# Kernel tuning notes

Hardware: AMD Instinct MI355X
Metric: run time of the kernel (lower is better)

## Reference

```python
import jax, jax.numpy as jnp
import numpy as np

B, H, W, Z = 2, 256, 256, 256


def _shift_zero(x, axis, offset):
    """Shift x along `axis` by `offset`, zero-filling the vacated slab.
    offset=-1: out[i] = x[i-1]; offset=+1: out[i] = x[i+1]."""
    pad = [(0, 0)] * x.ndim
    idx = [slice(None)] * x.ndim
    if offset == -1:
        pad[axis] = (1, 0)
        idx[axis] = slice(0, x.shape[axis])
    else:
        pad[axis] = (0, 1)
        idx[axis] = slice(1, x.shape[axis] + 1)
    return jnp.pad(x, pad)[tuple(idx)]


def apply_7pt_stencil(x, coeff):
    # x: [B,H,W,Z], coeff: [B,H,W,7] broadcast over Z
    west = _shift_zero(x, 2, -1)
    east = _shift_zero(x, 2, 1)
    south = _shift_zero(x, 1, -1)
    north = _shift_zero(x, 1, 1)
    bottom = _shift_zero(x, 3, -1)
    top = _shift_zero(x, 3, 1)
    c = coeff[..., None, :]  # [B,H,W,1,7]
    return (c[..., 0] * west + c[..., 1] * east + c[..., 2] * south
            + c[..., 3] * north + c[..., 4] * bottom + c[..., 5] * top
            + c[..., 6] * x)


def setup_inputs() -> dict:
    key = jax.random.key(0)
    k1, k2, k3 = jax.random.split(key, 3)
    x = jax.random.normal(k1, (B, H, W, Z), dtype=jnp.float32)
    coeff = jax.random.uniform(k2, (B, H, W, 7), dtype=jnp.float32)
    ref = jax.random.normal(k3, (B, H, W, Z), dtype=jnp.float32)
    return {"x": x, "coeff": coeff, "ref": ref}


def reference(x, coeff, ref):
    output = apply_7pt_stencil(x, coeff)
    error = (output - ref).astype(jnp.float32)
    loss = jnp.mean(error * error)
    max_abs_error = jnp.max(jnp.abs(error))
    return loss, output, max_abs_error
```

## Files before the change

kernel.cpp:

```cpp
#include <hip/hip_runtime.h>

#define HH 256
#define WW 256
#define ZZ 256
#define BBH 512
#define LSTRIDE (WW * ZZ)
#define NROWS (BBH * WW)
#define NELEM ((long long)NROWS * ZZ)

#define SEGW 8
#define NTW (WW / SEGW)
#define NPAIR (BBH / 2)
#define NSEG (NPAIR * NTW)
#define WPB 4
#define NBLK (NSEG / WPB)

typedef float vf4 __attribute__((ext_vector_type(4)));

__device__ __forceinline__ vf4 ld4(const float* p) { return *(const vf4*)p; }
__device__ __forceinline__ vf4 ldnt4(const float* p) {
    return __builtin_nontemporal_load((const vf4*)p);
}

__device__ __forceinline__ void store_row(float* rowp, vf4 o, int lane) {
    const float nx = __shfl_down(o.x, 1);
    const float ny = __shfl_down(o.y, 1);
    const float nz = __shfl_down(o.z, 1);
    if (lane < 63) {
        vf4 st = {o.w, nx, ny, nz};
        __builtin_nontemporal_store(st, (vf4*)(rowp + 4 * (lane + 1)));
    }
    if (lane == 0) {
        __builtin_nontemporal_store(o.x, rowp + 1);
        __builtin_nontemporal_store(o.y, rowp + 2);
        __builtin_nontemporal_store(o.z, rowp + 3);
    }
    if (lane == 63) __builtin_nontemporal_store(o.w, rowp + ZZ);
}

__global__ __launch_bounds__(256) void stencil7_kernel(
    const float* __restrict__ x, const float* __restrict__ coeff,
    const float* __restrict__ ref, float* __restrict__ outD,
    float* __restrict__ part_sum, float* __restrict__ part_max)
{
    const int tid  = threadIdx.x;
    const int k    = tid >> 6;
    const int lane = tid & 63;
    const int seg  = __builtin_amdgcn_readfirstlane(blockIdx.x * WPB + k);
    const int p    = seg >> 5;
    const int wt   = seg & (NTW - 1);
    const int bh0  = p * 2;
    const int w0   = wt * SEGW;
    const int h0   = bh0 & (HH - 1);
    const bool hasS = (h0 > 0);
    const bool hasN = (h0 != HH - 2);
    const long long SOFF = hasS ? -(long long)LSTRIDE : 0;
    const long long NOFF = hasN ? 2LL * LSTRIDE : (long long)LSTRIDE;
    const int lo = lane << 2;

    const float* px0  = x   + (long long)(bh0 * WW + w0) * ZZ + lo;
    const float* px1  = px0 + LSTRIDE;
    const float* prf0 = ref + (long long)(bh0 * WW + w0) * ZZ + lo;
    const float* prf1 = prf0 + LSTRIDE;
    const float* pc0  = coeff + 7LL * (bh0 * WW + w0);
    const float* pc1  = pc0 + 7 * WW;
    float* prow0 = outD + (long long)(bh0 * WW + w0) * ZZ;
    float* prow1 = prow0 + LSTRIDE;

    const vf4 z4 = {0.f, 0.f, 0.f, 0.f};

    vf4 cw0, cw1;
    if (w0 > 0) { cw0 = ld4(px0 - ZZ); cw1 = ld4(px1 - ZZ); }
    else        { cw0 = z4;            cw1 = z4; }
    vf4 c00 = ld4(px0);           vf4 c10 = ld4(px1);
    vf4 c01 = ld4(px0 + ZZ);      vf4 c11 = ld4(px1 + ZZ);
    vf4 sC  = ld4(px0 + SOFF);    vf4 nC  = ld4(px0 + NOFF);
    vf4 rf0 = ldnt4(prf0);        vf4 rf1 = ldnt4(prf1);
    float k0 = pc0[0], k1 = pc0[1], k2 = hasS ? pc0[2] : 0.f, k3 = pc0[3],
          k4 = pc0[4], k5 = pc0[5], k6 = pc0[6];
    float j0 = pc1[0], j1 = pc1[1], j2 = pc1[2], j3 = hasN ? pc1[3] : 0.f,
          j4 = pc1[4], j5 = pc1[5], j6 = pc1[6];

    float acc_s = 0.f, acc_m = 0.f;

    #pragma unroll
    for (int i = 0; i < SEGW - 1; ++i) {
        int ce = w0 + i + 2; if (ce > WW - 1) ce = WW - 1;
        const long long ceo = (long long)(ce - w0) * ZZ;
        vf4 c0n = ld4(px0 + ceo);
        vf4 c1n = ld4(px1 + ceo);
        const long long r1o = (long long)(i + 1) * ZZ;
        vf4 sN  = ld4(px0 + r1o + SOFF);
        vf4 nN  = ld4(px0 + r1o + NOFF);
        vf4 rf0n = ldnt4(prf0 + r1o);
        vf4 rf1n = ldnt4(prf1 + r1o);
        const float* qc0 = pc0 + 7 * (i + 1);
        const float* qc1 = pc1 + 7 * (i + 1);
        const float m0 = qc0[0], m1 = qc0[1], m2 = hasS ? qc0[2] : 0.f,
                    m3 = qc0[3], m4 = qc0[4], m5 = qc0[5], m6 = qc0[6];
        const float n0 = qc1[0], n1 = qc1[1], n2 = qc1[2],
                    n3 = hasN ? qc1[3] : 0.f, n4 = qc1[4], n5 = qc1[5], n6 = qc1[6];

        {
            float bm1 = __shfl_up(c00.w, 1);
            if (lane == 0) bm1 = 0.f;
            float tp1 = __shfl_down(c00.x, 1);
            if (lane == 63) tp1 = 0.f;
            const vf4 bot = {bm1, c00.x, c00.y, c00.z};
            const vf4 top = {c00.y, c00.z, c00.w, tp1};
            const vf4 o = k0*cw0 + k1*c01 + k2*sC + k3*c10 + k4*bot + k5*top + k6*c00;
            store_row(prow0 + (long long)i * ZZ, o, lane);
            const vf4 e = o - rf0;
            acc_s += e.x*e.x + e.y*e.y + e.z*e.z + e.w*e.w;
            acc_m  = fmaxf(acc_m, fmaxf(fmaxf(fabsf(e.x), fabsf(e.y)),
                                        fmaxf(fabsf(e.z), fabsf(e.w))));
        }
        {
            float bm1 = __shfl_up(c10.w, 1);
            if (lane == 0) bm1 = 0.f;
            float tp1 = __shfl_down(c10.x, 1);
            if (lane == 63) tp1 = 0.f;
            const vf4 bot = {bm1, c10.x, c10.y, c10.z};
            const vf4 top = {c10.y, c10.z, c10.w, tp1};
            const vf4 o = j0*cw1 + j1*c11 + j2*c00 + j3*nC + j4*bot + j5*top + j6*c10;
            store_row(prow1 + (long long)i * ZZ, o, lane);
            const vf4 e = o - rf1;
            acc_s += e.x*e.x + e.y*e.y + e.z*e.z + e.w*e.w;
            acc_m  = fmaxf(acc_m, fmaxf(fmaxf(fabsf(e.x), fabsf(e.y)),
                                        fmaxf(fabsf(e.z), fabsf(e.w))));
        }

        cw0 = c00; c00 = c01; c01 = c0n;
        cw1 = c10; c10 = c11; c11 = c1n;
        sC = sN; nC = nN; rf0 = rf0n; rf1 = rf1n;
        k0 = m0; k1 = m1; k2 = m2; k3 = m3; k4 = m4; k5 = m5; k6 = m6;
        j0 = n0; j1 = n1; j2 = n2; j3 = n3; j4 = n4; j5 = n5; j6 = n6;
    }

    {
        const int i = SEGW - 1;
        if (w0 + i == WW - 1) { k1 = 0.f; j1 = 0.f; }
        {
            float bm1 = __shfl_up(c00.w, 1);
            if (lane == 0) bm1 = 0.f;
            float tp1 = __shfl_down(c00.x, 1);
            if (lane == 63) tp1 = 0.f;
            const vf4 bot = {bm1, c00.x, c00.y, c00.z};
            const vf4 top = {c00.y, c00.z, c00.w, tp1};
            const vf4 o = k0*cw0 + k1*c01 + k2*sC + k3*c10 + k4*bot + k5*top + k6*c00;
            store_row(prow0 + (long long)i * ZZ, o, lane);
            const vf4 e = o - rf0;
            acc_s += e.x*e.x + e.y*e.y + e.z*e.z + e.w*e.w;
            acc_m  = fmaxf(acc_m, fmaxf(fmaxf(fabsf(e.x), fabsf(e.y)),
                                        fmaxf(fabsf(e.z), fabsf(e.w))));
        }
        {
            float bm1 = __shfl_up(c10.w, 1);
            if (lane == 0) bm1 = 0.f;
            float tp1 = __shfl_down(c10.x, 1);
            if (lane == 63) tp1 = 0.f;
            const vf4 bot = {bm1, c10.x, c10.y, c10.z};
            const vf4 top = {c10.y, c10.z, c10.w, tp1};
            const vf4 o = j0*cw1 + j1*c11 + j2*c00 + j3*nC + j4*bot + j5*top + j6*c10;
            store_row(prow1 + (long long)i * ZZ, o, lane);
            const vf4 e = o - rf1;
            acc_s += e.x*e.x + e.y*e.y + e.z*e.z + e.w*e.w;
            acc_m  = fmaxf(acc_m, fmaxf(fmaxf(fabsf(e.x), fabsf(e.y)),
                                        fmaxf(fabsf(e.z), fabsf(e.w))));
        }
    }

    #pragma unroll
    for (int off = 32; off > 0; off >>= 1) {
        acc_s += __shfl_down(acc_s, off);
        acc_m  = fmaxf(acc_m, __shfl_down(acc_m, off));
    }
    __shared__ float ss[WPB];
    __shared__ float sm[WPB];
    if (lane == 0) { ss[k] = acc_s; sm[k] = acc_m; }
    __syncthreads();
    if (tid == 0) {
        part_sum[blockIdx.x] = ss[0] + ss[1] + ss[2] + ss[3];
        part_max[blockIdx.x] = fmaxf(fmaxf(sm[0], sm[1]), fmaxf(sm[2], sm[3]));
    }
}

__global__ __launch_bounds__(256) void finalize_kernel(
    const float* __restrict__ part_sum, const float* __restrict__ part_max,
    float* __restrict__ loss_out, float* __restrict__ amax_out)
{
    const int tid  = threadIdx.x;
    const int wave = tid >> 6;
    const int lane = tid & 63;

    double s = 0.0;
    float  m = 0.f;
    for (int i = tid; i < NBLK; i += 256) {
        s += (double)part_sum[i];
        m  = fmaxf(m, part_max[i]);
    }
    #pragma unroll
    for (int off = 32; off > 0; off >>= 1) {
        s += __shfl_down(s, off);
        m  = fmaxf(m, __shfl_down(m, off));
    }
    __shared__ double ds[4];
    __shared__ float  dm[4];
    if (lane == 0) { ds[wave] = s; dm[wave] = m; }
    __syncthreads();
    if (tid == 0) {
        const double S = ds[0] + ds[1] + ds[2] + ds[3];
        const float  M = fmaxf(fmaxf(dm[0], dm[1]), fmaxf(dm[2], dm[3]));
        *loss_out = (float)(S / (double)NELEM);
        *amax_out = M;
    }
}

extern "C" void kernel_launch(void* const* d_in, const int* in_sizes, int n_in,
                              void* d_out, int out_size, void* d_ws, size_t ws_size,
                              hipStream_t stream) {
    const float* x     = (const float*)d_in[0];
    const float* coeff = (const float*)d_in[1];
    const float* ref   = (const float*)d_in[2];

    float* outf = (float*)d_out;
    float* loss_out = outf;
    float* amax_out = outf + 1 + NELEM;

    float* part_sum = (float*)d_ws;
    float* part_max = part_sum + NBLK;

    stencil7_kernel<<<dim3(NBLK), dim3(256), 0, stream>>>(
        x, coeff, ref, outf, part_sum, part_max);
    finalize_kernel<<<dim3(1), dim3(256), 0, stream>>>(
        part_sum, part_max, loss_out, amax_out);
}
```

Before: 74.49 us.

## Convert stencil kernel to persistent grid with atomic work-stealing task queue

```diff
diff --git a/kernel.cpp b/kernel.cpp
--- a/kernel.cpp
+++ b/kernel.cpp
@@ -13,7 +13,8 @@
 #define NPAIR (BBH / 2)
 #define NSEG (NPAIR * NTW)
 #define WPB 4
-#define NBLK (NSEG / WPB)
+#define NTASK (NSEG / WPB)
+#define GRIDP 1280
 
 typedef float vf4 __attribute__((ext_vector_type(4)));
 
@@ -41,147 +42,150 @@
 __global__ __launch_bounds__(256) void stencil7_kernel(
     const float* __restrict__ x, const float* __restrict__ coeff,
     const float* __restrict__ ref, float* __restrict__ outD,
+    unsigned int* __restrict__ ctr,
     float* __restrict__ part_sum, float* __restrict__ part_max)
 {
+    __shared__ int s_task;
     const int tid  = threadIdx.x;
     const int k    = tid >> 6;
     const int lane = tid & 63;
-    const int seg  = __builtin_amdgcn_readfirstlane(blockIdx.x * WPB + k);
-    const int p    = seg >> 5;
-    const int wt   = seg & (NTW - 1);
-    const int bh0  = p * 2;
-    const int w0   = wt * SEGW;
-    const int h0   = bh0 & (HH - 1);
-    const bool hasS = (h0 > 0);
-    const bool hasN = (h0 != HH - 2);
-    const long long SOFF = hasS ? -(long long)LSTRIDE : 0;
-    const long long NOFF = hasN ? 2LL * LSTRIDE : (long long)LSTRIDE;
-    const int lo = lane << 2;
-
-    const float* px0  = x   + (long long)(bh0 * WW + w0) * ZZ + lo;
-    const float* px1  = px0 + LSTRIDE;
-    const float* prf0 = ref + (long long)(bh0 * WW + w0) * ZZ + lo;
-    const float* prf1 = prf0 + LSTRIDE;
-    const float* pc0  = coeff + 7LL * (bh0 * WW + w0);
-    const float* pc1  = pc0 + 7 * WW;
-    float* prow0 = outD + (long long)(bh0 * WW + w0) * ZZ;
-    float* prow1 = prow0 + LSTRIDE;
-
+    const int lo   = lane << 2;
     const vf4 z4 = {0.f, 0.f, 0.f, 0.f};
 
-    vf4 cw0, cw1;
-    if (w0 > 0) { cw0 = ld4(px0 - ZZ); cw1 = ld4(px1 - ZZ); }
-    else        { cw0 = z4;            cw1 = z4; }
-    vf4 c00 = ld4(px0);           vf4 c10 = ld4(px1);
-    vf4 c01 = ld4(px0 + ZZ);      vf4 c11 = ld4(px1 + ZZ);
-    vf4 sC  = ld4(px0 + SOFF);    vf4 nC  = ld4(px0 + NOFF);
-    vf4 rf0 = ldnt4(prf0);        vf4 rf1 = ldnt4(prf1);
-    float k0 = pc0[0], k1 = pc0[1], k2 = hasS ? pc0[2] : 0.f, k3 = pc0[3],
-          k4 = pc0[4], k5 = pc0[5], k6 = pc0[6];
-    float j0 = pc1[0], j1 = pc1[1], j2 = pc1[2], j3 = hasN ? pc1[3] : 0.f,
-          j4 = pc1[4], j5 = pc1[5], j6 = pc1[6];
-
-    float acc_s = 0.f, acc_m = 0.f;
-
-    #pragma unroll
-    for (int i = 0; i < SEGW - 1; ++i) {
-        int ce = w0 + i + 2; if (ce > WW - 1) ce = WW - 1;
-        const long long ceo = (long long)(ce - w0) * ZZ;
-        vf4 c0n = ld4(px0 + ceo);
-        vf4 c1n = ld4(px1 + ceo);
-        const long long r1o = (long long)(i + 1) * ZZ;
-        vf4 sN  = ld4(px0 + r1o + SOFF);
-        vf4 nN  = ld4(px0 + r1o + NOFF);
-        vf4 rf0n = ldnt4(prf0 + r1o);
-        vf4 rf1n = ldnt4(prf1 + r1o);
-        const float* qc0 = pc0 + 7 * (i + 1);
-        const float* qc1 = pc1 + 7 * (i + 1);
-        const float m0 = qc0[0], m1 = qc0[1], m2 = hasS ? qc0[2] : 0.f,
-                    m3 = qc0[3], m4 = qc0[4], m5 = qc0[5], m6 = qc0[6];
-        const float n0 = qc1[0], n1 = qc1[1], n2 = qc1[2],
-                    n3 = hasN ? qc1[3] : 0.f, n4 = qc1[4], n5 = qc1[5], n6 = qc1[6];
+    int task = blockIdx.x;
+    while (task < NTASK) {
+        const int seg  = __builtin_amdgcn_readfirstlane(task * WPB + k);
+        const int p    = seg >> 5;
+        const int wt   = seg & (NTW - 1);
+        const int bh0  = p * 2;
+        const int w0   = wt * SEGW;
+        const int h0   = bh0 & (HH - 1);
+        const bool hasS = (h0 > 0);
+        const bool hasN = (h0 != HH - 2);
+        const long long SOFF = hasS ? -(long long)LSTRIDE : 0;
+        const long long NOFF = hasN ? 2LL * LSTRIDE : (long long)LSTRIDE;
+
+        const float* px0  = x   + (long long)(bh0 * WW + w0) * ZZ + lo;
+        const float* px1  = px0 + LSTRIDE;
+        const float* prf0 = ref + (long long)(bh0 * WW + w0) * ZZ + lo;
+        const float* prf1 = prf0 + LSTRIDE;
+        const float* pc0  = coeff + 7LL * (bh0 * WW + w0);
+        const float* pc1  = pc0 + 7 * WW;
+        float* prow0 = outD + (long long)(bh0 * WW + w0) * ZZ;
+        float* prow1 = prow0 + LSTRIDE;
+
+        vf4 cw0, cw1;
+        if (w0 > 0) { cw0 = ld4(px0 - ZZ); cw1 = ld4(px1 - ZZ); }
+        else        { cw0 = z4;            cw1 = z4; }
+        vf4 c00 = ld4(px0);           vf4 c10 = ld4(px1);
+        vf4 c01 = ld4(px0 + ZZ);      vf4 c11 = ld4(px1 + ZZ);
+        vf4 sC  = ld4(px0 + SOFF);    vf4 nC  = ld4(px0 + NOFF);
+        vf4 rf0 = ldnt4(prf0);        vf4 rf1 = ldnt4(prf1);
+        float k0 = pc0[0], k1 = pc0[1], k2 = hasS ? pc0[2] : 0.f, k3 = pc0[3],
+              k4 = pc0[4], k5 = pc0[5], k6 = pc0[6];
+        float j0 = pc1[0], j1 = pc1[1], j2 = pc1[2], j3 = hasN ? pc1[3] : 0.f,
+              j4 = pc1[4], j5 = pc1[5], j6 = pc1[6];
+
+        float acc_s = 0.f, acc_m = 0.f;
+
+        #pragma unroll
+        for (int i = 0; i < SEGW - 1; ++i) {
+            int ce = w0 + i + 2; if (ce > WW - 1) ce = WW - 1;
+            const long long ceo = (long long)(ce - w0) * ZZ;
+            vf4 c0n = ld4(px0 + ceo);
+            vf4 c1n = ld4(px1 + ceo);
+            const long long r1o = (long long)(i + 1) * ZZ;
+            vf4 sN  = ld4(px0 + r1o + SOFF);
+            vf4 nN  = ld4(px0 + r1o + NOFF);
+            vf4 rf0n = ldnt4(prf0 + r1o);
+            vf4 rf1n = ldnt4(prf1 + r1o);
+            const float* qc0 = pc0 + 7 * (i + 1);
+            const float* qc1 = pc1 + 7 * (i + 1);
+            const float m0 = qc0[0], m1 = qc0[1], m2 = hasS ? qc0[2] : 0.f,
+                        m3 = qc0[3], m4 = qc0[4], m5 = qc0[5], m6 = qc0[6];
+            const float n0 = qc1[0], n1 = qc1[1], n2 = qc1[2],
+                        n3 = hasN ? qc1[3] : 0.f, n4 = qc1[4], n5 = qc1[5], n6 = qc1[6];
+
+            {
+                float bm1 = __shfl_up(c00.w, 1);
+                if (lane == 0) bm1 = 0.f;
+                float tp1 = __shfl_down(c00.x, 1);
+                if (lane == 63) tp1 = 0.f;
+                const vf4 bot = {bm1, c00.x, c00.y, c00.z};
+                const vf4 top = {c00.y, c00.z, c00.w, tp1};
+                const vf4 o = k0*cw0 + k1*c01 + k2*sC + k3*c10 + k4*bot + k5*top + k6*c00;
+                store_row(prow0 + (long long)i * ZZ, o, lane);
+                const vf4 e = o - rf0;
+                acc_s += e.x*e.x + e.y*e.y + e.z*e.z + e.w*e.w;
+                acc_m  = fmaxf(acc_m, fmaxf(fmaxf(fabsf(e.x), fabsf(e.y)),
+                                            fmaxf(fabsf(e.z), fabsf(e.w))));
+            }
+            {
+                float bm1 = __shfl_up(c10.w, 1);
+                if (lane == 0) bm1 = 0.f;
+                float tp1 = __shfl_down(c10.x, 1);
+                if (lane == 63) tp1 = 0.f;
+                const vf4 bot = {bm1, c10.x, c10.y, c10.z};
+                const vf4 top = {c10.y, c10.z, c10.w, tp1};
+                const vf4 o = j0*cw1 + j1*c11 + j2*c00 + j3*nC + j4*bot + j5*top + j6*c10;
+                store_row(prow1 + (long long)i * ZZ, o, lane);
+                const vf4 e = o - rf1;
+                acc_s += e.x*e.x + e.y*e.y + e.z*e.z + e.w*e.w;
+                acc_m  = fmaxf(acc_m, fmaxf(fmaxf(fabsf(e.x), fabsf(e.y)),
+                                            fmaxf(fabsf(e.z), fabsf(e.w))));
+            }
+
+            cw0 = c00; c00 = c01; c01 = c0n;
+            cw1 = c10; c10 = c11; c11 = c1n;
+            sC = sN; nC = nN; rf0 = rf0n; rf1 = rf1n;
+            k0 = m0; k1 = m1; k2 = m2; k3 = m3; k4 = m4; k5 = m5; k6 = m6;
+            j0 = n0; j1 = n1; j2 = n2; j3 = n3; j4 = n4; j5 = n5; j6 = n6;
+        }
 
         {
-            float bm1 = __shfl_up(c00.w, 1);
-            if (lane == 0) bm1 = 0.f;
-            float tp1 = __shfl_down(c00.x, 1);
-            if (lane == 63) tp1 = 0.f;
-            const vf4 bot = {bm1, c00.x, c00.y, c00.z};
-            const vf4 top = {c00.y, c00.z, c00.w, tp1};
-            const vf4 o = k0*cw0 + k1*c01 + k2*sC + k3*c10 + k4*bot + k5*top + k6*c00;
-            store_row(prow0 + (long long)i * ZZ, o, lane);
-            const vf4 e = o - rf0;
-            acc_s += e.x*e.x + e.y*e.y + e.z*e.z + e.w*e.w;
-            acc_m  = fmaxf(acc_m, fmaxf(fmaxf(fabsf(e.x), fabsf(e.y)),
-                                        fmaxf(fabsf(e.z), fabsf(e.w))));
+            const int i = SEGW - 1;
+            if (w0 + i == WW - 1) { k1 = 0.f; j1 = 0.f; }
+            {
+                float bm1 = __shfl_up(c00.w, 1);
+                if (lane == 0) bm1 = 0.f;
+                float tp1 = __shfl_down(c00.x, 1);
+                if (lane == 63) tp1 = 0.f;
+                const vf4 bot = {bm1, c00.x, c00.y, c00.z};
+                const vf4 top = {c00.y, c00.z, c00.w, tp1};
+                const vf4 o = k0*cw0 + k1*c01 + k2*sC + k3*c10 + k4*bot + k5*top + k6*c00;
+                store_row(prow0 + (long long)i * ZZ, o, lane);
+                const vf4 e = o - rf0;
+                acc_s += e.x*e.x + e.y*e.y + e.z*e.z + e.w*e.w;
+                acc_m  = fmaxf(acc_m, fmaxf(fmaxf(fabsf(e.x), fabsf(e.y)),
+                                            fmaxf(fabsf(e.z), fabsf(e.w))));
+            }
+            {
+                float bm1 = __shfl_up(c10.w, 1);
+                if (lane == 0) bm1 = 0.f;
+                float tp1 = __shfl_down(c10.x, 1);
+                if (lane == 63) tp1 = 0.f;
+                const vf4 bot = {bm1, c10.x, c10.y, c10.z};
+                const vf4 top = {c10.y, c10.z, c10.w, tp1};
+                const vf4 o = j0*cw1 + j1*c11 + j2*c00 + j3*nC + j4*bot + j5*top + j6*c10;
+                store_row(prow1 + (long long)i * ZZ, o, lane);
+                const vf4 e = o - rf1;
+                acc_s += e.x*e.x + e.y*e.y + e.z*e.z + e.w*e.w;
+                acc_m  = fmaxf(acc_m, fmaxf(fmaxf(fabsf(e.x), fabsf(e.y)),
+                                            fmaxf(fabsf(e.z), fabsf(e.w))));
+            }
         }
-        {
-            float bm1 = __shfl_up(c10.w, 1);
-            if (lane == 0) bm1 = 0.f;
-            float tp1 = __shfl_down(c10.x, 1);
-            if (lane == 63) tp1 = 0.f;
-            const vf4 bot = {bm1, c10.x, c10.y, c10.z};
-            const vf4 top = {c10.y, c10.z, c10.w, tp1};
-            const vf4 o = j0*cw1 + j1*c11 + j2*c00 + j3*nC + j4*bot + j5*top + j6*c10;
-            store_row(prow1 + (long long)i * ZZ, o, lane);
-            const vf4 e = o - rf1;
-            acc_s += e.x*e.x + e.y*e.y + e.z*e.z + e.w*e.w;
-            acc_m  = fmaxf(acc_m, fmaxf(fmaxf(fabsf(e.x), fabsf(e.y)),
-                                        fmaxf(fabsf(e.z), fabsf(e.w))));
+
+        #pragma unroll
+        for (int off = 32; off > 0; off >>= 1) {
+            acc_s += __shfl_down(acc_s, off);
+            acc_m  = fmaxf(acc_m, __shfl_down(acc_m, off));
         }
-
-        cw0 = c00; c00 = c01; c01 = c0n;
-        cw1 = c10; c10 = c11; c11 = c1n;
-        sC = sN; nC = nN; rf0 = rf0n; rf1 = rf1n;
-        k0 = m0; k1 = m1; k2 = m2; k3 = m3; k4 = m4; k5 = m5; k6 = m6;
-        j0 = n0; j1 = n1; j2 = n2; j3 = n3; j4 = n4; j5 = n5; j6 = n6;
-    }
-
-    {
-        const int i = SEGW - 1;
-        if (w0 + i == WW - 1) { k1 = 0.f; j1 = 0.f; }
-        {
-            float bm1 = __shfl_up(c00.w, 1);
-            if (lane == 0) bm1 = 0.f;
-            float tp1 = __shfl_down(c00.x, 1);
-            if (lane == 63) tp1 = 0.f;
-            const vf4 bot = {bm1, c00.x, c00.y, c00.z};
-            const vf4 top = {c00.y, c00.z, c00.w, tp1};
-            const vf4 o = k0*cw0 + k1*c01 + k2*sC + k3*c10 + k4*bot + k5*top + k6*c00;
-            store_row(prow0 + (long long)i * ZZ, o, lane);
-            const vf4 e = o - rf0;
-            acc_s += e.x*e.x + e.y*e.y + e.z*e.z + e.w*e.w;
-            acc_m  = fmaxf(acc_m, fmaxf(fmaxf(fabsf(e.x), fabsf(e.y)),
-                                        fmaxf(fabsf(e.z), fabsf(e.w))));
-        }
-        {
-            float bm1 = __shfl_up(c10.w, 1);
-            if (lane == 0) bm1 = 0.f;
-            float tp1 = __shfl_down(c10.x, 1);
-            if (lane == 63) tp1 = 0.f;
-            const vf4 bot = {bm1, c10.x, c10.y, c10.z};
-            const vf4 top = {c10.y, c10.z, c10.w, tp1};
-            const vf4 o = j0*cw1 + j1*c11 + j2*c00 + j3*nC + j4*bot + j5*top + j6*c10;
-            store_row(prow1 + (long long)i * ZZ, o, lane);
-            const vf4 e = o - rf1;
-            acc_s += e.x*e.x + e.y*e.y + e.z*e.z + e.w*e.w;
-            acc_m  = fmaxf(acc_m, fmaxf(fmaxf(fabsf(e.x), fabsf(e.y)),
-                                        fmaxf(fabsf(e.z), fabsf(e.w))));
-        }
-    }
-
-    #pragma unroll
-    for (int off = 32; off > 0; off >>= 1) {
-        acc_s += __shfl_down(acc_s, off);
-        acc_m  = fmaxf(acc_m, __shfl_down(acc_m, off));
-    }
-    __shared__ float ss[WPB];
-    __shared__ float sm[WPB];
-    if (lane == 0) { ss[k] = acc_s; sm[k] = acc_m; }
-    __syncthreads();
-    if (tid == 0) {
-        part_sum[blockIdx.x] = ss[0] + ss[1] + ss[2] + ss[3];
-        part_max[blockIdx.x] = fmaxf(fmaxf(sm[0], sm[1]), fmaxf(sm[2], sm[3]));
+        if (lane == 0) { part_sum[seg] = acc_s; part_max[seg] = acc_m; }
+
+        __syncthreads();
+        if (tid == 0) s_task = GRIDP + (int)atomicAdd(ctr, 1u);
+        __syncthreads();
+        task = s_task;
     }
 }
 
@@ -195,7 +199,7 @@
 
     double s = 0.0;
     float  m = 0.f;
-    for (int i = tid; i < NBLK; i += 256) {
+    for (int i = tid; i < NSEG; i += 256) {
         s += (double)part_sum[i];
         m  = fmaxf(m, part_max[i]);
     }
@@ -227,11 +231,14 @@
     float* loss_out = outf;
     float* amax_out = outf + 1 + NELEM;
 
-    float* part_sum = (float*)d_ws;
-    float* part_max = part_sum + NBLK;
-
-    stencil7_kernel<<<dim3(NBLK), dim3(256), 0, stream>>>(
-        x, coeff, ref, outf, part_sum, part_max);
+    unsigned int* ctr = (unsigned int*)d_ws;
+    float* part_sum = (float*)((char*)d_ws + 256);
+    float* part_max = part_sum + NSEG;
+
+    hipMemsetAsync(ctr, 0, 4, stream);
+
+    stencil7_kernel<<<dim3(GRIDP), dim3(256), 0, stream>>>(
+        x, coeff, ref, outf, ctr, part_sum, part_max);
     finalize_kernel<<<dim3(1), dim3(256), 0, stream>>>(
         part_sum, part_max, loss_out, amax_out);
 }
```

Result: slower. 91.87 us (+23.3%).

## Deepen register prefetch to two rows ahead and remap blocks across XCDs

Applied to the files above, without the earlier changes.

```diff
diff --git a/kernel.cpp b/kernel.cpp
--- a/kernel.cpp
+++ b/kernel.cpp
@@ -14,6 +14,8 @@
 #define NSEG (NPAIR * NTW)
 #define WPB 4
 #define NBLK (NSEG / WPB)
+#define NXCD 8
+#define CPX (NBLK / NXCD)
 
 typedef float vf4 __attribute__((ext_vector_type(4)));
 
@@ -46,7 +48,9 @@
     const int tid  = threadIdx.x;
     const int k    = tid >> 6;
     const int lane = tid & 63;
-    const int seg  = __builtin_amdgcn_readfirstlane(blockIdx.x * WPB + k);
+    const int b    = blockIdx.x;
+    const int sb   = (b & (NXCD - 1)) * CPX + (b >> 3);
+    const int seg  = __builtin_amdgcn_readfirstlane(sb * WPB + k);
     const int p    = seg >> 5;
     const int wt   = seg & (NTW - 1);
     const int bh0  = p * 2;
@@ -69,104 +73,96 @@
 
     const vf4 z4 = {0.f, 0.f, 0.f, 0.f};
 
-    vf4 cw0, cw1;
-    if (w0 > 0) { cw0 = ld4(px0 - ZZ); cw1 = ld4(px1 - ZZ); }
-    else        { cw0 = z4;            cw1 = z4; }
-    vf4 c00 = ld4(px0);           vf4 c10 = ld4(px1);
-    vf4 c01 = ld4(px0 + ZZ);      vf4 c11 = ld4(px1 + ZZ);
-    vf4 sC  = ld4(px0 + SOFF);    vf4 nC  = ld4(px0 + NOFF);
-    vf4 rf0 = ldnt4(prf0);        vf4 rf1 = ldnt4(prf1);
-    float k0 = pc0[0], k1 = pc0[1], k2 = hasS ? pc0[2] : 0.f, k3 = pc0[3],
-          k4 = pc0[4], k5 = pc0[5], k6 = pc0[6];
-    float j0 = pc1[0], j1 = pc1[1], j2 = pc1[2], j3 = hasN ? pc1[3] : 0.f,
-          j4 = pc1[4], j5 = pc1[5], j6 = pc1[6];
+    vf4 W0, W1;
+    if (w0 > 0) { W0 = ld4(px0 - ZZ); W1 = ld4(px1 - ZZ); }
+    else        { W0 = z4;            W1 = z4; }
+    vf4 C0 = ld4(px0);            vf4 C1 = ld4(px1);
+    vf4 E0 = ld4(px0 + ZZ);       vf4 E1 = ld4(px1 + ZZ);
+    vf4 F0 = ld4(px0 + 2 * ZZ);   vf4 F1 = ld4(px1 + 2 * ZZ);
+    vf4 sA = ld4(px0 + SOFF);     vf4 nA = ld4(px0 + NOFF);
+    vf4 sB = ld4(px0 + ZZ + SOFF); vf4 nB = ld4(px0 + ZZ + NOFF);
+    vf4 rA0 = ldnt4(prf0);        vf4 rA1 = ldnt4(prf1);
+    vf4 rB0 = ldnt4(prf0 + ZZ);   vf4 rB1 = ldnt4(prf1 + ZZ);
+    float kA0 = pc0[0], kA1 = pc0[1], kA2 = hasS ? pc0[2] : 0.f, kA3 = pc0[3],
+          kA4 = pc0[4], kA5 = pc0[5], kA6 = pc0[6];
+    float jA0 = pc1[0], jA1 = pc1[1], jA2 = pc1[2], jA3 = hasN ? pc1[3] : 0.f,
+          jA4 = pc1[4], jA5 = pc1[5], jA6 = pc1[6];
+    float kB0 = pc0[7], kB1 = pc0[8], kB2 = hasS ? pc0[9] : 0.f, kB3 = pc0[10],
+          kB4 = pc0[11], kB5 = pc0[12], kB6 = pc0[13];
+    float jB0 = pc1[7], jB1 = pc1[8], jB2 = pc1[9], jB3 = hasN ? pc1[10] : 0.f,
+          jB4 = pc1[11], jB5 = pc1[12], jB6 = pc1[13];
 
     float acc_s = 0.f, acc_m = 0.f;
 
     #pragma unroll
-    for (int i = 0; i < SEGW - 1; ++i) {
-        int ce = w0 + i + 2; if (ce > WW - 1) ce = WW - 1;
-        const long long ceo = (long long)(ce - w0) * ZZ;
-        vf4 c0n = ld4(px0 + ceo);
-        vf4 c1n = ld4(px1 + ceo);
-        const long long r1o = (long long)(i + 1) * ZZ;
-        vf4 sN  = ld4(px0 + r1o + SOFF);
-        vf4 nN  = ld4(px0 + r1o + NOFF);
-        vf4 rf0n = ldnt4(prf0 + r1o);
-        vf4 rf1n = ldnt4(prf1 + r1o);
-        const float* qc0 = pc0 + 7 * (i + 1);
-        const float* qc1 = pc1 + 7 * (i + 1);
-        const float m0 = qc0[0], m1 = qc0[1], m2 = hasS ? qc0[2] : 0.f,
-                    m3 = qc0[3], m4 = qc0[4], m5 = qc0[5], m6 = qc0[6];
-        const float n0 = qc1[0], n1 = qc1[1], n2 = qc1[2],
-                    n3 = hasN ? qc1[3] : 0.f, n4 = qc1[4], n5 = qc1[5], n6 = qc1[6];
+    for (int i = 0; i < SEGW; ++i) {
+        vf4 sT = z4, nT = z4, rT0 = z4, rT1 = z4;
+        float kT0 = 0.f, kT1 = 0.f, kT2 = 0.f, kT3 = 0.f, kT4 = 0.f, kT5 = 0.f, kT6 = 0.f;
+        float jT0 = 0.f, jT1 = 0.f, jT2 = 0.f, jT3 = 0.f, jT4 = 0.f, jT5 = 0.f, jT6 = 0.f;
+        if (i + 2 < SEGW) {
+            const long long go = (long long)(i + 2) * ZZ;
+            sT  = ld4(px0 + go + SOFF);
+            nT  = ld4(px0 + go + NOFF);
+            rT0 = ldnt4(prf0 + go);
+            rT1 = ldnt4(prf1 + go);
+            const float* qc0 = pc0 + 7 * (i + 2);
+            const float* qc1 = pc1 + 7 * (i + 2);
+            kT0 = qc0[0]; kT1 = qc0[1]; kT2 = hasS ? qc0[2] : 0.f; kT3 = qc0[3];
+            kT4 = qc0[4]; kT5 = qc0[5]; kT6 = qc0[6];
+            jT0 = qc1[0]; jT1 = qc1[1]; jT2 = qc1[2]; jT3 = hasN ? qc1[3] : 0.f;
+            jT4 = qc1[4]; jT5 = qc1[5]; jT6 = qc1[6];
+        }
+        vf4 nF0 = z4, nF1 = z4;
+        if (i <= SEGW - 3) {
+            int wf = w0 + i + 3; if (wf > WW - 1) wf = WW - 1;
+            const long long fo = (long long)(wf - w0) * ZZ;
+            nF0 = ld4(px0 + fo);
+            nF1 = ld4(px1 + fo);
+        }
+
+        if (i == SEGW - 1) {
+            if (w0 + i == WW - 1) { kA1 = 0.f; jA1 = 0.f; }
+        }
 
         {
-            float bm1 = __shfl_up(c00.w, 1);
+            float bm1 = __shfl_up(C0.w, 1);
             if (lane == 0) bm1 = 0.f;
-            float tp1 = __shfl_down(c00.x, 1);
+            float tp1 = __shfl_down(C0.x, 1);
             if (lane == 63) tp1 = 0.f;
-            const vf4 bot = {bm1, c00.x, c00.y, c00.z};
-            const vf4 top = {c00.y, c00.z, c00.w, tp1};
-            const vf4 o = k0*cw0 + k1*c01 + k2*sC + k3*c10 + k4*bot + k5*top + k6*c00;
+            const vf4 bot = {bm1, C0.x, C0.y, C0.z};
+            const vf4 top = {C0.y, C0.z, C0.w, tp1};
+            const vf4 o = kA0*W0 + kA1*E0 + kA2*sA + kA3*C1 + kA4*bot + kA5*top + kA6*C0;
             store_row(prow0 + (long long)i * ZZ, o, lane);
-            const vf4 e = o - rf0;
+            const vf4 e = o - rA0;
             acc_s += e.x*e.x + e.y*e.y + e.z*e.z + e.w*e.w;
             acc_m  = fmaxf(acc_m, fmaxf(fmaxf(fabsf(e.x), fabsf(e.y)),
                                         fmaxf(fabsf(e.z), fabsf(e.w))));
         }
         {
-            float bm1 = __shfl_up(c10.w, 1);
+            float bm1 = __shfl_up(C1.w, 1);
             if (lane == 0) bm1 = 0.f;
-            float tp1 = __shfl_down(c10.x, 1);
+            float tp1 = __shfl_down(C1.x, 1);
             if (lane == 63) tp1 = 0.f;
-            const vf4 bot = {bm1, c10.x, c10.y, c10.z};
-            const vf4 top = {c10.y, c10.z, c10.w, tp1};
-            const vf4 o = j0*cw1 + j1*c11 + j2*c00 + j3*nC + j4*bot + j5*top + j6*c10;
+            const vf4 bot = {bm1, C1.x, C1.y, C1.z};
+            const vf4 top = {C1.y, C1.z, C1.w, tp1};
+            const vf4 o = jA0*W1 + jA1*E1 + jA2*C0 + jA3*nA + jA4*bot + jA5*top + jA6*C1;
             store_row(prow1 + (long long)i * ZZ, o, lane);
-            const vf4 e = o - rf1;
+            const vf4 e = o - rA1;
             acc_s += e.x*e.x + e.y*e.y + e.z*e.z + e.w*e.w;
             acc_m  = fmaxf(acc_m, fmaxf(fmaxf(fabsf(e.x), fabsf(e.y)),
                                         fmaxf(fabsf(e.z), fabsf(e.w))));
         }
 
-        cw0 = c00; c00 = c01; c01 = c0n;
-        cw1 = c10; c10 = c11; c11 = c1n;
-        sC = sN; nC = nN; rf0 = rf0n; rf1 = rf1n;
-        k0 = m0; k1 = m1; k2 = m2; k3 = m3; k4 = m4; k5 = m5; k6 = m6;
-        j0 = n0; j1 = n1; j2 = n2; j3 = n3; j4 = n4; j5 = n5; j6 = n6;
-    }
-
-    {
-        const int i = SEGW - 1;
-        if (w0 + i == WW - 1) { k1 = 0.f; j1 = 0.f; }
-        {
-            float bm1 = __shfl_up(c00.w, 1);
-            if (lane == 0) bm1 = 0.f;
-            float tp1 = __shfl_down(c00.x, 1);
-            if (lane == 63) tp1 = 0.f;
-            const vf4 bot = {bm1, c00.x, c00.y, c00.z};
-            const vf4 top = {c00.y, c00.z, c00.w, tp1};
-            const vf4 o = k0*cw0 + k1*c01 + k2*sC + k3*c10 + k4*bot + k5*top + k6*c00;
-            store_row(prow0 + (long long)i * ZZ, o, lane);
-            const vf4 e = o - rf0;
-            acc_s += e.x*e.x + e.y*e.y + e.z*e.z + e.w*e.w;
-            acc_m  = fmaxf(acc_m, fmaxf(fmaxf(fabsf(e.x), fabsf(e.y)),
-                                        fmaxf(fabsf(e.z), fabsf(e.w))));
-        }
-        {
-            float bm1 = __shfl_up(c10.w, 1);
-            if (lane == 0) bm1 = 0.f;
-            float tp1 = __shfl_down(c10.x, 1);
-            if (lane == 63) tp1 = 0.f;
-            const vf4 bot = {bm1, c10.x, c10.y, c10.z};
-            const vf4 top = {c10.y, c10.z, c10.w, tp1};
-            const vf4 o = j0*cw1 + j1*c11 + j2*c00 + j3*nC + j4*bot + j5*top + j6*c10;
-            store_row(prow1 + (long long)i * ZZ, o, lane);
-            const vf4 e = o - rf1;
-            acc_s += e.x*e.x + e.y*e.y + e.z*e.z + e.w*e.w;
-            acc_m  = fmaxf(acc_m, fmaxf(fmaxf(fabsf(e.x), fabsf(e.y)),
-                                        fmaxf(fabsf(e.z), fabsf(e.w))));
+        W0 = C0; C0 = E0; E0 = F0;
+        W1 = C1; C1 = E1; E1 = F1;
+        if (i <= SEGW - 3) { F0 = nF0; F1 = nF1; }
+        sA = sB; nA = nB; rA0 = rB0; rA1 = rB1;
+        kA0 = kB0; kA1 = kB1; kA2 = kB2; kA3 = kB3; kA4 = kB4; kA5 = kB5; kA6 = kB6;
+        jA0 = jB0; jA1 = jB1; jA2 = jB2; jA3 = jB3; jA4 = jB4; jA5 = jB5; jA6 = jB6;
+        if (i + 2 < SEGW) {
+            sB = sT; nB = nT; rB0 = rT0; rB1 = rT1;
+            kB0 = kT0; kB1 = kT1; kB2 = kT2; kB3 = kT3; kB4 = kT4; kB5 = kT5; kB6 = kT6;
+            jB0 = jT0; jB1 = jT1; jB2 = jT2; jB3 = jT3; jB4 = jT4; jB5 = jT5; jB6 = jT6;
         }
     }
 
```

Measured after the change: 88.69 us. 19.1% more time.
